# Optimization experiments

Hardware: AMD Instinct MI355X
Metric: run time of the kernel (lower is better)

The kernel has to match this reference:

```python
import jax, jax.numpy as jnp
import numpy as np

E = 256      # embedding_dim
H = 16       # head_num
D = 16       # qkv_dim
FF = 512     # ff_hidden_dim
L = 5        # encoder_layer_num
B = 4        # batch
N = 256      # node_cnt
EPS = 1e-5   # InstanceNorm eps


def setup_inputs() -> dict:
    key = jax.random.key(0)
    ks = jax.random.split(key, 16)
    s = 0.05

    def nrm(k, shape):
        return jax.random.normal(k, shape, dtype=jnp.float32) * s

    return {
        "data": jax.random.normal(ks[0], (B, N, N), dtype=jnp.float32),
        "node_rand": jax.random.uniform(ks[1], (B, N, 1), dtype=jnp.float32),
        # Cross_Encoder input projections (Linear(1, E))
        "Wnode": nrm(ks[2], (1, E)), "bnode": jnp.zeros((E,), jnp.float32),
        "Wedge": nrm(ks[3], (1, E)), "bedge": jnp.zeros((E,), jnp.float32),
        # Per layer (L) x per block (2: row/col) weights
        "Wq": nrm(ks[4], (L, 2, E, H * D)),
        "Wk": nrm(ks[5], (L, 2, E, H * D)),
        "Wv": nrm(ks[6], (L, 2, E, H * D)),
        "Wcomb": nrm(ks[7], (L, 2, H * D, E)),
        "bcomb": jnp.zeros((L, 2, E), jnp.float32),
        "n1w": jnp.ones((L, 2, E), jnp.float32),
        "n1b": jnp.zeros((L, 2, E), jnp.float32),
        "W1": nrm(ks[8], (L, 2, E, FF)),
        "b1": jnp.zeros((L, 2, FF), jnp.float32),
        "W2": nrm(ks[9], (L, 2, FF, E)),
        "b2": jnp.zeros((L, 2, E), jnp.float32),
        "n2w": jnp.ones((L, 2, E), jnp.float32),
        "n2b": jnp.zeros((L, 2, E), jnp.float32),
        # MixedScore edge-bias projection per block: E -> H channels
        "Wmix": nrm(ks[10], (L, 2, E, H)),
    }


def _instance_norm(x, w, b):
    # x: [B, N, E]; InstanceNorm1d after transpose -> normalize over node dim N per (B, channel)
    mu = jnp.mean(x, axis=1, keepdims=True)
    var = jnp.var(x, axis=1, keepdims=True)
    return (x - mu) * jax.lax.rsqrt(var + EPS) * w + b


def reference(data, node_rand, Wnode, bnode, Wedge, bedge,
              Wq, Wk, Wv, Wcomb, bcomb, n1w, n1b,
              W1, b1, W2, b2, n2w, n2b, Wmix):
    inv_sqrt_d = jnp.float32(1.0) / jnp.sqrt(jnp.float32(D))

    def block(row, col, edge, i, j):
        # row, col: [B, N, E]; edge: [B, N, N, E]
        q = (row @ Wq[i, j]).reshape(B, N, H, D)
        k = (col @ Wk[i, j]).reshape(B, N, H, D)
        v = (col @ Wv[i, j]).reshape(B, N, H, D)
        score = jnp.einsum('bnhd,bmhd->bhnm', q, k) * inv_sqrt_d
        score = score + jnp.einsum('bnme,eh->bhnm', edge, Wmix[i, j])
        w = jax.nn.softmax(score, axis=-1)
        out = jnp.einsum('bhnm,bmhd->bnhd', w, v).reshape(B, N, H * D)
        mh = out @ Wcomb[i, j] + bcomb[i, j]
        o1 = _instance_norm(row + mh, n1w[i, j], n1b[i, j])
        ff = jax.nn.relu(o1 @ W1[i, j] + b1[i, j]) @ W2[i, j] + b2[i, j]
        return _instance_norm(o1 + ff, n2w[i, j], n2b[i, j])

    # compute_normalized_matrices: per-batch global min-max scaling
    flat = data.reshape(B, -1)
    mn = flat.min(axis=1).reshape(B, 1, 1)
    mx = flat.max(axis=1).reshape(B, 1, 1)
    rng = mx - mn
    rng = jnp.where(rng == 0, jnp.float32(1.0), rng)
    scaled = (data - mn) / rng

    edge = scaled[..., None] @ Wedge + bedge           # [B, N, N, E]
    emb = node_rand @ Wnode + bnode                    # [B, N, E]

    row, col = emb, emb
    for i in range(L):
        row_new = block(row, col, edge, i, 0)
        col = block(col, row, jnp.swapaxes(edge, 1, 2), i, 1)
        row = row_new
    return row, col
```

## Files before the change

kernel.cpp:

```cpp
#include <hip/hip_runtime.h>
#include <hip/hip_bf16.h>

#define E 256
#define H 16
#define DD 16
#define FFH 512
#define LAYERS 5
#define BB 4
#define NN 256
#define MROWS 1024

typedef __attribute__((ext_vector_type(8))) short bfrag;
typedef __attribute__((ext_vector_type(4))) float f32x4;
typedef __attribute__((ext_vector_type(8))) unsigned short us8;
typedef unsigned short u16;

__device__ __forceinline__ void bsplit(float v, u16& h, u16& l) {
    unsigned u = __float_as_uint(v);
    u16 hh = (u16)((u + 0x7fffu + ((u >> 16) & 1u)) >> 16);
    float r = v - __uint_as_float((unsigned)hh << 16);
    unsigned u2 = __float_as_uint(r);
    h = hh;
    l = (u16)((u2 + 0x7fffu + ((u2 >> 16) & 1u)) >> 16);
}

union PrepS {
    float tile[32 * 33];
    struct { u16 th[64 * 40], tl[64 * 40]; } wp;
    struct { float smin[4], smax[4]; } mm;
};

__global__ __launch_bounds__(256) void k_prep(
    const float* __restrict__ data, const float* __restrict__ node_rand,
    const float* __restrict__ Wnode, const float* __restrict__ bnode,
    const float* __restrict__ Wedge, const float* __restrict__ bedge,
    const float* __restrict__ Wmix,
    const float* __restrict__ Wq, const float* __restrict__ Wk, const float* __restrict__ Wv,
    const float* __restrict__ Wc, const float* __restrict__ W1, const float* __restrict__ W2,
    float* __restrict__ pmin, float* __restrict__ pmax, float* __restrict__ c1c0,
    float* __restrict__ rowb, float* __restrict__ colb,
    u16* rowh, u16* rowl, u16* colh, u16* coll,
    float* __restrict__ dataT,
    u16* qh, u16* ql, u16* kh, u16* kl_, u16* vh, u16* vl,
    u16* ch, u16* cl, u16* f1h, u16* f1l, u16* f2h, u16* f2l) {
    __shared__ PrepS ps;
    int bid = blockIdx.x;
    int t = threadIdx.x;
    if (bid < 64) {
        int b = bid >> 4, p = bid & 15;
        const float* src = data + (size_t)b * NN * NN + p * 4096;
        float lmin = 1e30f, lmax = -1e30f;
        #pragma unroll
        for (int i = 0; i < 16; i++) {
            float v = src[t + i * 256];
            lmin = fminf(lmin, v);
            lmax = fmaxf(lmax, v);
        }
        #pragma unroll
        for (int off = 32; off; off >>= 1) {
            lmin = fminf(lmin, __shfl_down(lmin, off));
            lmax = fmaxf(lmax, __shfl_down(lmax, off));
        }
        int wid = t >> 6, lane = t & 63;
        if (lane == 0) { ps.mm.smin[wid] = lmin; ps.mm.smax[wid] = lmax; }
        __syncthreads();
        if (t == 0) {
            pmin[b * 16 + p] = fminf(fminf(ps.mm.smin[0], ps.mm.smin[1]), fminf(ps.mm.smin[2], ps.mm.smin[3]));
            pmax[b * 16 + p] = fmaxf(fmaxf(ps.mm.smax[0], ps.mm.smax[1]), fmaxf(ps.mm.smax[2], ps.mm.smax[3]));
        }
    } else if (bid < 1088) {
        int idx = (bid - 64) * 256 + t;
        int bn = idx >> 8, e = idx & 255;
        float v = node_rand[bn] * Wnode[e] + bnode[e];
        rowb[idx] = v;
        colb[idx] = v;
        u16 h, l;
        bsplit(v, h, l);
        rowh[idx] = h; rowl[idx] = l;
        colh[idx] = h; coll[idx] = l;
    } else if (bid < 1344) {
        int local = bid - 1088;
        int bx = local & 7, by = (local >> 3) & 7, b = local >> 6;
        int r0 = by * 32, c0 = bx * 32;
        int tx = t & 31, ty = t >> 5;
        const float* src = data + (size_t)b * NN * NN;
        float* dst = dataT + (size_t)b * NN * NN;
        #pragma unroll
        for (int i = 0; i < 4; i++)
            ps.tile[(ty + 8 * i) * 33 + tx] = src[(size_t)(r0 + ty + 8 * i) * NN + c0 + tx];
        __syncthreads();
        #pragma unroll
        for (int i = 0; i < 4; i++)
            dst[(size_t)(c0 + ty + 8 * i) * NN + r0 + tx] = ps.tile[tx * 33 + ty + 8 * i];
    } else if (bid < 3904) {
        int id = bid - 1344;
        const float* W; u16 *Dh, *Dl; int K, N, mat, s, nt;
        if (id < 1280) {
            int seg = id / 320, local = id % 320;
            mat = local >> 5; int rem = local & 31; s = rem >> 2; nt = rem & 3;
            K = 256; N = 256;
            W  = seg == 0 ? Wq : seg == 1 ? Wk : seg == 2 ? Wv : Wc;
            Dh = seg == 0 ? qh : seg == 1 ? kh : seg == 2 ? vh : ch;
            Dl = seg == 0 ? ql : seg == 1 ? kl_ : seg == 2 ? vl : cl;
        } else if (id < 1920) {
            int local = id - 1280;
            mat = local >> 6; int rem = local & 63; s = rem >> 3; nt = rem & 7;
            K = 256; N = 512; W = W1; Dh = f1h; Dl = f1l;
        } else {
            int local = id - 1920;
            mat = local >> 6; int rem = local & 63; s = rem >> 2; nt = rem & 3;
            K = 512; N = 256; W = W2; Dh = f2h; Dl = f2l;
        }
        int kk = t >> 3, nl = (t & 7) * 8;
        const float* p = W + (size_t)mat * K * N + (size_t)(s * 32 + kk) * N + nt * 64 + nl;
        float4 f0 = *(const float4*)p;
        float4 f1v = *(const float4*)(p + 4);
        float fv[8] = {f0.x, f0.y, f0.z, f0.w, f1v.x, f1v.y, f1v.z, f1v.w};
        #pragma unroll
        for (int i = 0; i < 8; i++) bsplit(fv[i], ps.wp.th[(nl + i) * 40 + kk], ps.wp.tl[(nl + i) * 40 + kk]);
        __syncthreads();
        int n = t >> 2, ko = (t & 3) * 8;
        size_t dbase = (size_t)mat * K * N + (size_t)s * N * 32 + (size_t)nt * 64 * 32
                     + (size_t)n * 32 + ko;
        *(us8*)(Dh + dbase) = *(const us8*)&ps.wp.th[n * 40 + ko];
        *(us8*)(Dl + dbase) = *(const us8*)&ps.wp.tl[n * 40 + ko];
    } else {
        if (t < LAYERS * 2 * H) {
            int lj = t >> 4, h = t & 15;
            float c1 = 0.f, c0 = 0.f;
            for (int e = 0; e < E; e++) {
                float wm = Wmix[(lj * E + e) * H + h];
                c1 += Wedge[e] * wm;
                c0 += bedge[e] * wm;
            }
            c1c0[t] = c1;
            c1c0[160 + t] = c0;
        }
    }
}

__device__ __forceinline__ void mfma_gemm(const u16* __restrict__ Ah, const u16* __restrict__ Al,
                                          const u16* __restrict__ Bh, const u16* __restrict__ Bl,
                                          const float* __restrict__ bias, const float* __restrict__ R,
                                          float* __restrict__ Cf, u16* __restrict__ Ch,
                                          u16* __restrict__ Cl, int K, int Ncols, int relu) {
    __shared__ u16 AsH[32 * 136], AsL[32 * 136], BsH[64 * 136], BsL[64 * 136];
    int t = threadIdx.x;
    int lane = t & 63, wave = t >> 6;
    int quad = lane >> 4, l16 = lane & 15;
    int wy = wave >> 1, wx = wave & 1;
    int mBase = blockIdx.x * 32, nBase = blockIdx.y * 64;
    f32x4 acc0 = {0.f, 0.f, 0.f, 0.f}, acc1 = acc0;
    int arow = t >> 3, ak = (t & 7) * 16;
    int bcol = lane, bq = wave;
    const int nslab = K >> 7;
    const u16* apH = Ah + (size_t)(mBase + arow) * K + ak;
    const u16* apL = Al + (size_t)(mBase + arow) * K + ak;
    const size_t sstr = (size_t)Ncols * 32;
    size_t bbase = (size_t)bq * sstr + (size_t)(nBase + bcol) * 32;
    const u16* bpH = Bh + bbase;
    const u16* bpL = Bl + bbase;
    us8 rah0 = *(const us8*)apH, rah1 = *(const us8*)(apH + 8);
    us8 ral0 = *(const us8*)apL, ral1 = *(const us8*)(apL + 8);
    us8 rbh0 = *(const us8*)(bpH + 0);
    us8 rbh1 = *(const us8*)(bpH + 8);
    us8 rbh2 = *(const us8*)(bpH + 16);
    us8 rbh3 = *(const us8*)(bpH + 24);
    us8 rbl0 = *(const us8*)(bpL + 0);
    us8 rbl1 = *(const us8*)(bpL + 8);
    us8 rbl2 = *(const us8*)(bpL + 16);
    us8 rbl3 = *(const us8*)(bpL + 24);
    for (int s = 0; s < nslab; s++) {
        __syncthreads();
        *(us8*)&AsH[arow * 136 + ak] = rah0;  *(us8*)&AsH[arow * 136 + ak + 8] = rah1;
        *(us8*)&AsL[arow * 136 + ak] = ral0;  *(us8*)&AsL[arow * 136 + ak + 8] = ral1;
        {
            int bb = bcol * 136 + bq * 32;
            *(us8*)&BsH[bb + 0] = rbh0;  *(us8*)&BsH[bb + 8] = rbh1;
            *(us8*)&BsH[bb + 16] = rbh2; *(us8*)&BsH[bb + 24] = rbh3;
            *(us8*)&BsL[bb + 0] = rbl0;  *(us8*)&BsL[bb + 8] = rbl1;
            *(us8*)&BsL[bb + 16] = rbl2; *(us8*)&BsL[bb + 24] = rbl3;
        }
        __syncthreads();
        if (s + 1 < nslab) {
            rah0 = *(const us8*)(apH + (s + 1) * 128);
            rah1 = *(const us8*)(apH + (s + 1) * 128 + 8);
            ral0 = *(const us8*)(apL + (s + 1) * 128);
            ral1 = *(const us8*)(apL + (s + 1) * 128 + 8);
            const u16* nbH = bpH + (size_t)(4 * (s + 1)) * sstr;
            const u16* nbL = bpL + (size_t)(4 * (s + 1)) * sstr;
            rbh0 = *(const us8*)(nbH + 0);  rbh1 = *(const us8*)(nbH + 8);
            rbh2 = *(const us8*)(nbH + 16); rbh3 = *(const us8*)(nbH + 24);
            rbl0 = *(const us8*)(nbL + 0);  rbl1 = *(const us8*)(nbL + 8);
            rbl2 = *(const us8*)(nbL + 16); rbl3 = *(const us8*)(nbL + 24);
        }
        #pragma unroll
        for (int c = 0; c < 4; c++) {
            bfrag a_h = *(const bfrag*)&AsH[(wy * 16 + l16) * 136 + c * 32 + quad * 8];
            bfrag a_l = *(const bfrag*)&AsL[(wy * 16 + l16) * 136 + c * 32 + quad * 8];
            bfrag b_h0 = *(const bfrag*)&BsH[(wx * 32 + l16) * 136 + c * 32 + quad * 8];
            bfrag b_h1 = *(const bfrag*)&BsH[(wx * 32 + 16 + l16) * 136 + c * 32 + quad * 8];
            bfrag b_l0 = *(const bfrag*)&BsL[(wx * 32 + l16) * 136 + c * 32 + quad * 8];
            bfrag b_l1 = *(const bfrag*)&BsL[(wx * 32 + 16 + l16) * 136 + c * 32 + quad * 8];
            acc0 = __builtin_amdgcn_mfma_f32_16x16x32_bf16(a_h, b_h0, acc0, 0, 0, 0);
            acc1 = __builtin_amdgcn_mfma_f32_16x16x32_bf16(a_h, b_h1, acc1, 0, 0, 0);
            acc0 = __builtin_amdgcn_mfma_f32_16x16x32_bf16(a_h, b_l0, acc0, 0, 0, 0);
            acc1 = __builtin_amdgcn_mfma_f32_16x16x32_bf16(a_h, b_l1, acc1, 0, 0, 0);
            acc0 = __builtin_amdgcn_mfma_f32_16x16x32_bf16(a_l, b_h0, acc0, 0, 0, 0);
            acc1 = __builtin_amdgcn_mfma_f32_16x16x32_bf16(a_l, b_h1, acc1, 0, 0, 0);
        }
    }
    int col0 = nBase + wx * 32 + l16;
    int col1 = col0 + 16;
    float bia0 = bias ? bias[col0] : 0.f;
    float bia1 = bias ? bias[col1] : 0.f;
    #pragma unroll
    for (int r = 0; r < 4; r++) {
        int row0 = mBase + wy * 16 + quad * 4 + r;
        float v0 = acc0[r] + bia0, v1 = acc1[r] + bia1;
        if (R) {
            v0 += R[(size_t)row0 * Ncols + col0];
            v1 += R[(size_t)row0 * Ncols + col1];
        }
        if (relu) {
            v0 = fmaxf(v0, 0.f); v1 = fmaxf(v1, 0.f);
        }
        if (Cf) {
            Cf[(size_t)row0 * Ncols + col0] = v0;
            Cf[(size_t)row0 * Ncols + col1] = v1;
        } else {
            u16 h, l;
            bsplit(v0, h, l); Ch[(size_t)row0 * Ncols + col0] = h; Cl[(size_t)row0 * Ncols + col0] = l;
            bsplit(v1, h, l); Ch[(size_t)row0 * Ncols + col1] = h; Cl[(size_t)row0 * Ncols + col1] = l;
        }
    }
}

__global__ __launch_bounds__(256) void k_qkv(const u16* __restrict__ rowh, const u16* __restrict__ rowl,
                                             const u16* __restrict__ colh, const u16* __restrict__ coll,
                                             const u16* __restrict__ WqTh, const u16* __restrict__ WqTl,
                                             const u16* __restrict__ WkTh, const u16* __restrict__ WkTl,
                                             const u16* __restrict__ WvTh, const u16* __restrict__ WvTl,
                                             int lb2,
                                             float* q0, float* k0, float* v0,
                                             float* q1, float* k1, float* v1) {
    int z = blockIdx.z;
    int j = z / 3, w = z % 3;
    const u16* Ah = (w == 0) ? (j ? colh : rowh) : (j ? rowh : colh);
    const u16* Al = (w == 0) ? (j ? coll : rowl) : (j ? rowl : coll);
    const u16* Wh = (w == 0 ? WqTh : (w == 1 ? WkTh : WvTh)) + (size_t)(lb2 + j) * E * E;
    const u16* Wl = (w == 0 ? WqTl : (w == 1 ? WkTl : WvTl)) + (size_t)(lb2 + j) * E * E;
    float* outs[6] = {q0, k0, v0, q1, k1, v1};
    mfma_gemm(Ah, Al, Wh, Wl, nullptr, nullptr, outs[z], nullptr, nullptr, E, E, 0);
}

__global__ __launch_bounds__(256) void k_mgemm(const u16* Ah0, const u16* Al0,
                                               const u16* Ah1, const u16* Al1,
                                               const u16* __restrict__ Bh, const u16* __restrict__ Bl,
                                               int lb2, long wstride,
                                               const float* __restrict__ biasl, int bstride,
                                               const float* R0, const float* R1,
                                               float* Cf0, float* Cf1,
                                               u16* Ch0, u16* Cl0, u16* Ch1, u16* Cl1,
                                               int K, int Ncols, int relu) {
    int j = blockIdx.z;
    mfma_gemm(j ? Ah1 : Ah0, j ? Al1 : Al0,
              Bh + (size_t)(lb2 + j) * wstride, Bl + (size_t)(lb2 + j) * wstride,
              biasl ? biasl + (size_t)j * bstride : nullptr,
              R0 ? (j ? R1 : R0) : nullptr,
              Cf0 ? (j ? Cf1 : Cf0) : nullptr,
              Ch0 ? (j ? Ch1 : Ch0) : nullptr,
              Cl0 ? (j ? Cl1 : Cl0) : nullptr,
              K, Ncols, relu);
}

__global__ __launch_bounds__(256, 8) void k_attn(const float* __restrict__ q0, const float* __restrict__ k0,
                                                 const float* __restrict__ v0, const float* __restrict__ q1,
                                                 const float* __restrict__ k1, const float* __restrict__ v1,
                                                 const float* __restrict__ data, const float* __restrict__ dataT,
                                                 const float* __restrict__ pmin, const float* __restrict__ pmax,
                                                 const float* __restrict__ c1c0, int lj_base,
                                                 u16* __restrict__ atth0, u16* __restrict__ attl0,
                                                 u16* __restrict__ atth1, u16* __restrict__ attl1) {
    int wgid = blockIdx.x;
    int r8 = wgid & 7;
    int qd = wgid >> 3;
    int ng = qd & 15;
    int bhj = r8 * 16 + (qd >> 4);
    int bh = bhj >> 1;
    int j = bhj & 1;
    int b = bh >> 4, h = bh & 15;
    const float* q = j ? q1 : q0;
    const float* k = j ? k1 : k0;
    const float* v = j ? v1 : v0;
    float mn = 1e30f, mx = -1e30f;
    #pragma unroll
    for (int p = 0; p < 16; p++) {
        mn = fminf(mn, pmin[b * 16 + p]);
        mx = fmaxf(mx, pmax[b * 16 + p]);
    }
    float rng = mx - mn;
    if (rng == 0.f) rng = 1.f;
    float inv = 1.f / rng;
    float c1p = inv * c1c0[(lj_base + j) * 16 + h];
    float c0p = c1c0[160 + (lj_base + j) * 16 + h] - mn * c1p;

    __shared__ float kl[128 * 20];
    __shared__ float vl[128 * 20];
    int t = threadIdx.x;
    int lane = t & 63, w = t >> 6;
    int nq = lane >> 4;
    int dh = (lane >> 3) & 1;
    int ml = lane & 7;
    int n = ng * 16 + w * 4 + nq;

    float qr[8];
    {
        const float* qp = q + ((size_t)(b * NN + n) * E) + h * DD + dh * 8;
        float4 qa = *(const float4*)qp;
        float4 qb = *(const float4*)(qp + 4);
        qr[0] = qa.x; qr[1] = qa.y; qr[2] = qa.z; qr[3] = qa.w;
        qr[4] = qb.x; qr[5] = qb.y; qr[6] = qb.z; qr[7] = qb.w;
    }
    const float* pedge = (j ? dataT : data) + (size_t)b * NN * NN + (size_t)n * NN;

    float sum = 0.f;
    float acc[8] = {};
    int sc = t & 3, sr = t >> 2;
    for (int ph = 0; ph < 2; ph++) {
        if (ph) __syncthreads();
        #pragma unroll
        for (int it = 0; it < 2; it++) {
            int rl = sr + 64 * it;
            int mrow = ph * 128 + rl;
            const float* kp = k + ((size_t)(b * NN + mrow) * E) + h * DD + sc * 4;
            const float* vp = v + ((size_t)(b * NN + mrow) * E) + h * DD + sc * 4;
            *(float4*)&kl[rl * 20 + sc * 4] = *(const float4*)kp;
            *(float4*)&vl[rl * 20 + sc * 4] = *(const float4*)vp;
        }
        __syncthreads();
        #pragma unroll 4
        for (int i = 0; i < 16; i++) {
            int m = 8 * i + ml;
            float4 ka = *(const float4*)&kl[m * 20 + dh * 8];
            float4 kb = *(const float4*)&kl[m * 20 + dh * 8 + 4];
            float sA = (qr[0] * ka.x + qr[1] * ka.y + qr[2] * ka.z + qr[3] * ka.w)
                     + (qr[4] * kb.x + qr[5] * kb.y + qr[6] * kb.z + qr[7] * kb.w);
            float sB = __shfl_xor(sA, 8);
            float s = (sA + sB) * 0.25f + pedge[ph * 128 + m] * c1p + c0p;
            float e = __expf(s);
            sum += e;
            float4 va = *(const float4*)&vl[m * 20 + dh * 8];
            float4 vb = *(const float4*)&vl[m * 20 + dh * 8 + 4];
            acc[0] += e * va.x; acc[1] += e * va.y; acc[2] += e * va.z; acc[3] += e * va.w;
            acc[4] += e * vb.x; acc[5] += e * vb.y; acc[6] += e * vb.z; acc[7] += e * vb.w;
        }
    }
    #pragma unroll
    for (int mask = 1; mask <= 4; mask <<= 1) {
        sum += __shfl_xor(sum, mask);
        #pragma unroll
        for (int d = 0; d < 8; d++) acc[d] += __shfl_xor(acc[d], mask);
    }
    if (ml == 0) {
        float invs = 1.f / sum;
        u16 hh[8], ll[8];
        #pragma unroll
        for (int d = 0; d < 8; d++) bsplit(acc[d] * invs, hh[d], ll[d]);
        size_t base = ((size_t)(b * NN + n) * E) + h * DD + dh * 8;
        u16* oh = (j ? atth1 : atth0) + base;
        u16* ol = (j ? attl1 : attl0) + base;
        *(us8*)oh = *(const us8*)&hh[0];
        *(us8*)ol = *(const us8*)&ll[0];
    }
}

__global__ __launch_bounds__(256) void k_inorm(const float* __restrict__ Y0, const float* __restrict__ Y1,
                                               const float* __restrict__ wl, const float* __restrict__ bl,
                                               int pstride,
                                               float* Of0, float* Of1,
                                               u16* Oh0, u16* Ol0, u16* Oh1, u16* Ol1,
                                               float* __restrict__ fout) {
    int b = blockIdx.x, j = blockIdx.y;
    int ec = blockIdx.z * 8;
    const float* Y = (j ? Y1 : Y0) + (size_t)b * NN * E;
    float* O = (j ? Of1 : Of0) + (size_t)b * NN * E;
    u16* Oh = (j ? Oh1 : Oh0) + (size_t)b * NN * E;
    u16* Ol = (j ? Ol1 : Ol0) + (size_t)b * NN * E;
    const float* w = wl + (size_t)j * pstride;
    const float* bb = bl + (size_t)j * pstride;
    int t = threadIdx.x;
    int et = t & 7, n0 = t >> 3;
    int e = ec + et;
    float vals[8];
    float s = 0.f, s2 = 0.f;
    #pragma unroll
    for (int kk = 0; kk < 8; kk++) {
        float v = Y[(size_t)(n0 + 32 * kk) * E + e];
        vals[kk] = v;
        s += v;
        s2 += v * v;
    }
    __shared__ float ps[32 * 9], ps2[32 * 9];
    ps[n0 * 9 + et] = s;
    ps2[n0 * 9 + et] = s2;
    __syncthreads();
    float st = 0.f, st2 = 0.f;
    #pragma unroll
    for (int kk = 0; kk < 32; kk++) { st += ps[kk * 9 + et]; st2 += ps2[kk * 9 + et]; }
    float mu = st * (1.f / NN);
    float var = fmaxf(st2 * (1.f / NN) - mu * mu, 0.f);
    float scale = w[e] * rsqrtf(var + 1e-5f);
    float shift = bb[e] - mu * scale;
    #pragma unroll
    for (int kk = 0; kk < 8; kk++) {
        float vv = vals[kk] * scale + shift;
        size_t idx = (size_t)(n0 + 32 * kk) * E + e;
        O[idx] = vv;
        u16 hh, ll;
        bsplit(vv, hh, ll);
        Oh[idx] = hh;
        Ol[idx] = ll;
        if (fout) fout[(size_t)j * (BB * NN * E) + (size_t)b * NN * E + idx] = vv;
    }
}


extern "C" void kernel_launch(void* const* d_in, const int* in_sizes, int n_in,
                              void* d_out, int out_size, void* d_ws, size_t ws_size,
                              hipStream_t stream) {
    const float* data      = (const float*)d_in[0];
    const float* node_rand = (const float*)d_in[1];
    const float* Wnode     = (const float*)d_in[2];
    const float* bnode     = (const float*)d_in[3];
    const float* Wedge     = (const float*)d_in[4];
    const float* bedge     = (const float*)d_in[5];
    const float* Wq        = (const float*)d_in[6];
    const float* Wk        = (const float*)d_in[7];
    const float* Wv        = (const float*)d_in[8];
    const float* Wcomb     = (const float*)d_in[9];
    const float* bcomb     = (const float*)d_in[10];
    const float* n1w       = (const float*)d_in[11];
    const float* n1b       = (const float*)d_in[12];
    const float* W1        = (const float*)d_in[13];
    const float* b1        = (const float*)d_in[14];
    const float* W2        = (const float*)d_in[15];
    const float* b2        = (const float*)d_in[16];
    const float* n2w       = (const float*)d_in[17];
    const float* n2b       = (const float*)d_in[18];
    const float* Wmix      = (const float*)d_in[19];
    float* out = (float*)d_out;

    float* ws = (float*)d_ws;
    const size_t T = (size_t)MROWS * E;
    const size_t TF = (size_t)MROWS * FFH;
    float* dataT = ws + 0 * T;
    float* row   = ws + 1 * T;
    float* col   = ws + 2 * T;
    float* q0    = ws + 3 * T;
    float* q1    = ws + 4 * T;
    float* k0    = ws + 5 * T;
    float* k1    = ws + 6 * T;
    float* v0    = ws + 7 * T;
    float* v1    = ws + 8 * T;
    float* o1f0  = ws + 9 * T;
    float* o1f1  = ws + 10 * T;
    float* pmin  = ws + 11 * T;
    float* pmax  = pmin + 64;
    float* c1c0  = pmax + 64;
    u16* us = (u16*)(ws + 11 * T + 512);
    auto nxt = [&](size_t n) { u16* p = us; us += n; return p; };
    u16* rowh = nxt(T);  u16* rowl = nxt(T);
    u16* colh = nxt(T);  u16* coll = nxt(T);
    u16* atth0 = nxt(T); u16* attl0 = nxt(T);
    u16* atth1 = nxt(T); u16* attl1 = nxt(T);
    u16* o1h0 = nxt(T);  u16* o1l0 = nxt(T);
    u16* o1h1 = nxt(T);  u16* o1l1 = nxt(T);
    u16* ffhh0 = nxt(TF); u16* ffhl0 = nxt(TF);
    u16* ffhh1 = nxt(TF); u16* ffhl1 = nxt(TF);
    const size_t EE10 = (size_t)10 * E * E;
    const size_t EF10 = (size_t)10 * E * FFH;
    u16* WqTh = nxt(EE10); u16* WqTl = nxt(EE10);
    u16* WkTh = nxt(EE10); u16* WkTl = nxt(EE10);
    u16* WvTh = nxt(EE10); u16* WvTl = nxt(EE10);
    u16* WcTh = nxt(EE10); u16* WcTl = nxt(EE10);
    u16* W1Th = nxt(EF10); u16* W1Tl = nxt(EF10);
    u16* W2Th = nxt(EF10); u16* W2Tl = nxt(EF10);
    float* y0 = q0;   float* y1 = q1;
    float* y20 = q0;  float* y21 = q1;

    k_prep<<<3905, 256, 0, stream>>>(data, node_rand, Wnode, bnode,
                                     Wedge, bedge, Wmix,
                                     Wq, Wk, Wv, Wcomb, W1, W2,
                                     pmin, pmax, c1c0,
                                     row, col, rowh, rowl, colh, coll, dataT,
                                     WqTh, WqTl, WkTh, WkTl, WvTh, WvTl,
                                     WcTh, WcTl, W1Th, W1Tl, W2Th, W2Tl);

    for (int l = 0; l < LAYERS; l++) {
        int lb2 = l * 2;
        k_qkv<<<dim3(32, 4, 6), 256, 0, stream>>>(rowh, rowl, colh, coll,
                                                  WqTh, WqTl, WkTh, WkTl, WvTh, WvTl, lb2,
                                                  q0, k0, v0, q1, k1, v1);
        k_attn<<<dim3(2048), 256, 0, stream>>>(q0, k0, v0, q1, k1, v1, data, dataT,
                                               pmin, pmax, c1c0, lb2,
                                               atth0, attl0, atth1, attl1);
        k_mgemm<<<dim3(32, 4, 2), 256, 0, stream>>>(atth0, attl0, atth1, attl1,
                                                    WcTh, WcTl, lb2, (long)E * E,
                                                    bcomb, E,
                                                    row, col, y0, y1,
                                                    nullptr, nullptr, nullptr, nullptr,
                                                    E, E, 0);
        k_inorm<<<dim3(BB, 2, 32), 256, 0, stream>>>(y0, y1,
                                                     n1w + (size_t)lb2 * E, n1b + (size_t)lb2 * E, E,
                                                     o1f0, o1f1, o1h0, o1l0, o1h1, o1l1, nullptr);
        k_mgemm<<<dim3(32, 8, 2), 256, 0, stream>>>(o1h0, o1l0, o1h1, o1l1,
                                                    W1Th, W1Tl, lb2, (long)E * FFH,
                                                    b1, FFH,
                                                    nullptr, nullptr, nullptr, nullptr,
                                                    ffhh0, ffhl0, ffhh1, ffhl1,
                                                    E, FFH, 1);
        k_mgemm<<<dim3(32, 4, 2), 256, 0, stream>>>(ffhh0, ffhl0, ffhh1, ffhl1,
                                                    W2Th, W2Tl, lb2, (long)FFH * E,
                                                    b2, E,
                                                    o1f0, o1f1, q0 , q1 ,
                                                    nullptr, nullptr, nullptr, nullptr,
                                                    FFH, E, 0);
        k_inorm<<<dim3(BB, 2, 32), 256, 0, stream>>>(y20, y21,
                                                     n2w + (size_t)lb2 * E, n2b + (size_t)lb2 * E, E,
                                                     row, col, rowh, rowl, colh, coll,
                                                     (l == LAYERS - 1) ? out : nullptr);
    }
}
```

Baseline: 441.2 us.

## Move attention QK and PV products onto bf16 split-precision MFMA

```diff
diff --git a/kernel.cpp b/kernel.cpp
--- a/kernel.cpp
+++ b/kernel.cpp
@@ -242,16 +242,17 @@
                                              const u16* __restrict__ WkTh, const u16* __restrict__ WkTl,
                                              const u16* __restrict__ WvTh, const u16* __restrict__ WvTl,
                                              int lb2,
-                                             float* q0, float* k0, float* v0,
-                                             float* q1, float* k1, float* v1) {
+                                             u16* qhh0, u16* qhl0, u16* khh0, u16* khl0, u16* vhh0, u16* vhl0,
+                                             u16* qhh1, u16* qhl1, u16* khh1, u16* khl1, u16* vhh1, u16* vhl1) {
     int z = blockIdx.z;
     int j = z / 3, w = z % 3;
     const u16* Ah = (w == 0) ? (j ? colh : rowh) : (j ? rowh : colh);
     const u16* Al = (w == 0) ? (j ? coll : rowl) : (j ? rowl : coll);
     const u16* Wh = (w == 0 ? WqTh : (w == 1 ? WkTh : WvTh)) + (size_t)(lb2 + j) * E * E;
     const u16* Wl = (w == 0 ? WqTl : (w == 1 ? WkTl : WvTl)) + (size_t)(lb2 + j) * E * E;
-    float* outs[6] = {q0, k0, v0, q1, k1, v1};
-    mfma_gemm(Ah, Al, Wh, Wl, nullptr, nullptr, outs[z], nullptr, nullptr, E, E, 0);
+    u16* outs_h[6] = {qhh0, khh0, vhh0, qhh1, khh1, vhh1};
+    u16* outs_l[6] = {qhl0, khl0, vhl0, qhl1, khl1, vhl1};
+    mfma_gemm(Ah, Al, Wh, Wl, nullptr, nullptr, nullptr, outs_h[z], outs_l[z], E, E, 0);
 }
 
 __global__ __launch_bounds__(256) void k_mgemm(const u16* Ah0, const u16* Al0,
@@ -274,25 +275,37 @@
               K, Ncols, relu);
 }
 
-__global__ __launch_bounds__(256, 8) void k_attn(const float* __restrict__ q0, const float* __restrict__ k0,
-                                                 const float* __restrict__ v0, const float* __restrict__ q1,
-                                                 const float* __restrict__ k1, const float* __restrict__ v1,
-                                                 const float* __restrict__ data, const float* __restrict__ dataT,
-                                                 const float* __restrict__ pmin, const float* __restrict__ pmax,
-                                                 const float* __restrict__ c1c0, int lj_base,
-                                                 u16* __restrict__ atth0, u16* __restrict__ attl0,
-                                                 u16* __restrict__ atth1, u16* __restrict__ attl1) {
+__global__ __launch_bounds__(256) void k_attn(
+    const u16* __restrict__ qh0, const u16* __restrict__ ql0,
+    const u16* __restrict__ kh0, const u16* __restrict__ kl0,
+    const u16* __restrict__ vh0, const u16* __restrict__ vl0,
+    const u16* __restrict__ qh1, const u16* __restrict__ ql1,
+    const u16* __restrict__ kh1, const u16* __restrict__ kl1,
+    const u16* __restrict__ vh1, const u16* __restrict__ vl1,
+    const float* __restrict__ data, const float* __restrict__ dataT,
+    const float* __restrict__ pmin, const float* __restrict__ pmax,
+    const float* __restrict__ c1c0, int lj_base,
+    u16* __restrict__ atth0, u16* __restrict__ attl0,
+    u16* __restrict__ atth1, u16* __restrict__ attl1) {
+    __shared__ u16 Ks[256 * 56];
+    __shared__ u16 VTh[16 * 264];
+    __shared__ u16 VTl[16 * 264];
+    __shared__ u16 Pw[4][2 * 16 * 40];
+
     int wgid = blockIdx.x;
     int r8 = wgid & 7;
     int qd = wgid >> 3;
-    int ng = qd & 15;
-    int bhj = r8 * 16 + (qd >> 4);
+    int nq = qd & 3;
+    int bhj = r8 * 16 + (qd >> 2);
     int bh = bhj >> 1;
     int j = bhj & 1;
     int b = bh >> 4, h = bh & 15;
-    const float* q = j ? q1 : q0;
-    const float* k = j ? k1 : k0;
-    const float* v = j ? v1 : v0;
+    const u16* qh = j ? qh1 : qh0;
+    const u16* ql = j ? ql1 : ql0;
+    const u16* kh = j ? kh1 : kh0;
+    const u16* kl = j ? kl1 : kl0;
+    const u16* vh = j ? vh1 : vh0;
+    const u16* vl = j ? vl1 : vl0;
     float mn = 1e30f, mx = -1e30f;
     #pragma unroll
     for (int p = 0; p < 16; p++) {
@@ -305,74 +318,97 @@
     float c1p = inv * c1c0[(lj_base + j) * 16 + h];
     float c0p = c1c0[160 + (lj_base + j) * 16 + h] - mn * c1p;
 
-    __shared__ float kl[128 * 20];
-    __shared__ float vl[128 * 20];
     int t = threadIdx.x;
     int lane = t & 63, w = t >> 6;
-    int nq = lane >> 4;
-    int dh = (lane >> 3) & 1;
-    int ml = lane & 7;
-    int n = ng * 16 + w * 4 + nq;
-
-    float qr[8];
+    int l16 = lane & 15, g = lane >> 4;
+    int nb = nq * 64 + w * 16;
+    int n = nb + l16;
+
+    bfrag qbh, qbl;
     {
-        const float* qp = q + ((size_t)(b * NN + n) * E) + h * DD + dh * 8;
-        float4 qa = *(const float4*)qp;
-        float4 qb = *(const float4*)(qp + 4);
-        qr[0] = qa.x; qr[1] = qa.y; qr[2] = qa.z; qr[3] = qa.w;
-        qr[4] = qb.x; qr[5] = qb.y; qr[6] = qb.z; qr[7] = qb.w;
-    }
+        size_t qoff = ((size_t)(b * NN + n) * E) + h * DD + (g & 1) * 8;
+        qbh = *(const bfrag*)(qh + qoff);
+        qbl = *(const bfrag*)(ql + qoff);
+    }
+
+    {
+        size_t roff = ((size_t)(b * NN + t) * E) + h * DD;
+        us8 a = *(const us8*)(kh + roff);
+        us8 bv = *(const us8*)(kh + roff + 8);
+        us8 c = *(const us8*)(kl + roff);
+        us8 d = *(const us8*)(kl + roff + 8);
+        *(us8*)&Ks[t * 56 + 0] = a;   *(us8*)&Ks[t * 56 + 8] = bv;
+        *(us8*)&Ks[t * 56 + 16] = c;  *(us8*)&Ks[t * 56 + 24] = d;
+        us8 zz = (us8)(unsigned short)0;
+        *(us8*)&Ks[t * 56 + 32] = zz; *(us8*)&Ks[t * 56 + 40] = zz;
+        us8 vh0v = *(const us8*)(vh + roff);
+        us8 vh1v = *(const us8*)(vh + roff + 8);
+        us8 vl0v = *(const us8*)(vl + roff);
+        us8 vl1v = *(const us8*)(vl + roff + 8);
+        #pragma unroll
+        for (int d2 = 0; d2 < 8; d2++) {
+            VTh[d2 * 264 + t] = vh0v[d2];
+            VTh[(d2 + 8) * 264 + t] = vh1v[d2];
+            VTl[d2 * 264 + t] = vl0v[d2];
+            VTl[(d2 + 8) * 264 + t] = vl1v[d2];
+        }
+    }
+    __syncthreads();
+
     const float* pedge = (j ? dataT : data) + (size_t)b * NN * NN + (size_t)n * NN;
-
+    u16* myPh = &Pw[w][0];
+    u16* myPl = &Pw[w][16 * 40];
+    f32x4 oacc = {0.f, 0.f, 0.f, 0.f};
     float sum = 0.f;
-    float acc[8] = {};
-    int sc = t & 3, sr = t >> 2;
-    for (int ph = 0; ph < 2; ph++) {
-        if (ph) __syncthreads();
-        #pragma unroll
-        for (int it = 0; it < 2; it++) {
-            int rl = sr + 64 * it;
-            int mrow = ph * 128 + rl;
-            const float* kp = k + ((size_t)(b * NN + mrow) * E) + h * DD + sc * 4;
-            const float* vp = v + ((size_t)(b * NN + mrow) * E) + h * DD + sc * 4;
-            *(float4*)&kl[rl * 20 + sc * 4] = *(const float4*)kp;
-            *(float4*)&vl[rl * 20 + sc * 4] = *(const float4*)vp;
-        }
-        __syncthreads();
-        #pragma unroll 4
-        for (int i = 0; i < 16; i++) {
-            int m = 8 * i + ml;
-            float4 ka = *(const float4*)&kl[m * 20 + dh * 8];
-            float4 kb = *(const float4*)&kl[m * 20 + dh * 8 + 4];
-            float sA = (qr[0] * ka.x + qr[1] * ka.y + qr[2] * ka.z + qr[3] * ka.w)
-                     + (qr[4] * kb.x + qr[5] * kb.y + qr[6] * kb.z + qr[7] * kb.w);
-            float sB = __shfl_xor(sA, 8);
-            float s = (sA + sB) * 0.25f + pedge[ph * 128 + m] * c1p + c0p;
-            float e = __expf(s);
-            sum += e;
-            float4 va = *(const float4*)&vl[m * 20 + dh * 8];
-            float4 vb = *(const float4*)&vl[m * 20 + dh * 8 + 4];
-            acc[0] += e * va.x; acc[1] += e * va.y; acc[2] += e * va.z; acc[3] += e * va.w;
-            acc[4] += e * vb.x; acc[5] += e * vb.y; acc[6] += e * vb.z; acc[7] += e * vb.w;
-        }
-    }
+    int aoff1 = g * 8;
+    int aoff2 = g * 8 + ((g & 2) << 3);
+
+    for (int c = 0; c < 8; c++) {
+        #pragma unroll
+        for (int tt = 0; tt < 2; tt++) {
+            int mt = c * 2 + tt;
+            int mrow = mt * 16 + l16;
+            bfrag a1 = *(const bfrag*)&Ks[mrow * 56 + aoff1];
+            bfrag a2 = *(const bfrag*)&Ks[mrow * 56 + aoff2];
+            f32x4 sacc = {0.f, 0.f, 0.f, 0.f};
+            sacc = __builtin_amdgcn_mfma_f32_16x16x32_bf16(a1, qbh, sacc, 0, 0, 0);
+            sacc = __builtin_amdgcn_mfma_f32_16x16x32_bf16(a2, qbl, sacc, 0, 0, 0);
+            float4 ev = *(const float4*)&pedge[mt * 16 + g * 4];
+            float evf[4] = {ev.x, ev.y, ev.z, ev.w};
+            u16 ph[4], pl[4];
+            #pragma unroll
+            for (int r = 0; r < 4; r++) {
+                float s = sacc[r] * 0.25f + evf[r] * c1p + c0p;
+                float e = __expf(s);
+                sum += e;
+                bsplit(e, ph[r], pl[r]);
+            }
+            ushort4 phv; phv.x = ph[0]; phv.y = ph[1]; phv.z = ph[2]; phv.w = ph[3];
+            ushort4 plv; plv.x = pl[0]; plv.y = pl[1]; plv.z = pl[2]; plv.w = pl[3];
+            *(ushort4*)&myPh[l16 * 40 + tt * 16 + g * 4] = phv;
+            *(ushort4*)&myPl[l16 * 40 + tt * 16 + g * 4] = plv;
+        }
+        bfrag pbh = *(const bfrag*)&myPh[l16 * 40 + g * 8];
+        bfrag pbl = *(const bfrag*)&myPl[l16 * 40 + g * 8];
+        bfrag vah = *(const bfrag*)&VTh[l16 * 264 + c * 32 + g * 8];
+        bfrag vaL = *(const bfrag*)&VTl[l16 * 264 + c * 32 + g * 8];
+        oacc = __builtin_amdgcn_mfma_f32_16x16x32_bf16(vah, pbh, oacc, 0, 0, 0);
+        oacc = __builtin_amdgcn_mfma_f32_16x16x32_bf16(vah, pbl, oacc, 0, 0, 0);
+        oacc = __builtin_amdgcn_mfma_f32_16x16x32_bf16(vaL, pbh, oacc, 0, 0, 0);
+    }
+    sum += __shfl_xor(sum, 16);
+    sum += __shfl_xor(sum, 32);
+    float invs = 1.f / sum;
+    u16 hh[4], ll[4];
     #pragma unroll
-    for (int mask = 1; mask <= 4; mask <<= 1) {
-        sum += __shfl_xor(sum, mask);
-        #pragma unroll
-        for (int d = 0; d < 8; d++) acc[d] += __shfl_xor(acc[d], mask);
-    }
-    if (ml == 0) {
-        float invs = 1.f / sum;
-        u16 hh[8], ll[8];
-        #pragma unroll
-        for (int d = 0; d < 8; d++) bsplit(acc[d] * invs, hh[d], ll[d]);
-        size_t base = ((size_t)(b * NN + n) * E) + h * DD + dh * 8;
-        u16* oh = (j ? atth1 : atth0) + base;
-        u16* ol = (j ? attl1 : attl0) + base;
-        *(us8*)oh = *(const us8*)&hh[0];
-        *(us8*)ol = *(const us8*)&ll[0];
-    }
+    for (int r = 0; r < 4; r++) bsplit(oacc[r] * invs, hh[r], ll[r]);
+    size_t obase = ((size_t)(b * NN + n) * E) + h * DD + g * 4;
+    u16* oh = (j ? atth1 : atth0) + obase;
+    u16* ol = (j ? attl1 : attl0) + obase;
+    ushort4 ohv; ohv.x = hh[0]; ohv.y = hh[1]; ohv.z = hh[2]; ohv.w = hh[3];
+    ushort4 olv; olv.x = ll[0]; olv.y = ll[1]; olv.z = ll[2]; olv.w = ll[3];
+    *(ushort4*)oh = ohv;
+    *(ushort4*)ol = olv;
 }
 
 __global__ __launch_bounds__(256) void k_inorm(const float* __restrict__ Y0, const float* __restrict__ Y1,
@@ -459,10 +495,6 @@
     float* col   = ws + 2 * T;
     float* q0    = ws + 3 * T;
     float* q1    = ws + 4 * T;
-    float* k0    = ws + 5 * T;
-    float* k1    = ws + 6 * T;
-    float* v0    = ws + 7 * T;
-    float* v1    = ws + 8 * T;
     float* o1f0  = ws + 9 * T;
     float* o1f1  = ws + 10 * T;
     float* pmin  = ws + 11 * T;
@@ -486,6 +518,12 @@
     u16* WcTh = nxt(EE10); u16* WcTl = nxt(EE10);
     u16* W1Th = nxt(EF10); u16* W1Tl = nxt(EF10);
     u16* W2Th = nxt(EF10); u16* W2Tl = nxt(EF10);
+    u16* qhh0 = nxt(T); u16* qhl0 = nxt(T);
+    u16* khh0 = nxt(T); u16* khl0 = nxt(T);
+    u16* vhh0 = nxt(T); u16* vhl0 = nxt(T);
+    u16* qhh1 = nxt(T); u16* qhl1 = nxt(T);
+    u16* khh1 = nxt(T); u16* khl1 = nxt(T);
+    u16* vhh1 = nxt(T); u16* vhl1 = nxt(T);
     float* y0 = q0;   float* y1 = q1;
     float* y20 = q0;  float* y21 = q1;
 
@@ -501,10 +539,12 @@
         int lb2 = l * 2;
         k_qkv<<<dim3(32, 4, 6), 256, 0, stream>>>(rowh, rowl, colh, coll,
                                                   WqTh, WqTl, WkTh, WkTl, WvTh, WvTl, lb2,
-                                                  q0, k0, v0, q1, k1, v1);
-        k_attn<<<dim3(2048), 256, 0, stream>>>(q0, k0, v0, q1, k1, v1, data, dataT,
-                                               pmin, pmax, c1c0, lb2,
-                                               atth0, attl0, atth1, attl1);
+                                                  qhh0, qhl0, khh0, khl0, vhh0, vhl0,
+                                                  qhh1, qhl1, khh1, khl1, vhh1, vhl1);
+        k_attn<<<dim3(512), 256, 0, stream>>>(qhh0, qhl0, khh0, khl0, vhh0, vhl0,
+                                              qhh1, qhl1, khh1, khl1, vhh1, vhl1,
+                                              data, dataT, pmin, pmax, c1c0, lb2,
+                                              atth0, attl0, atth1, attl1);
         k_mgemm<<<dim3(32, 4, 2), 256, 0, stream>>>(atth0, attl0, atth1, attl1,
                                                     WcTh, WcTl, lb2, (long)E * E,
                                                     bcomb, E,
```

After: 367.9 us. 1.2x faster.
